# Performance work log

Measured on AMD Instinct MI355X. Metric: run time of the kernel, lower is better.

Reference implementation:

```python
import math
import jax, jax.numpy as jnp
import numpy as np

B, N, L, D, H = 1, 64, 512, 768, 12
DK = D // H


def setup_inputs() -> dict:
    rng = jax.random.key(0)
    ks = jax.random.split(rng, 8)
    s = 0.02  # weight init scale
    return {
        "query": jax.random.normal(ks[0], (B, N, L, D), jnp.float32),
        "key": jax.random.normal(ks[1], (B, N, L, D), jnp.float32),
        "value": jax.random.normal(ks[2], (B, N, L, D), jnp.float32),
        "Wq": jax.random.normal(ks[3], (D, D), jnp.float32) * s,
        "bq": jnp.zeros((D,), jnp.float32),
        "Wk": jax.random.normal(ks[4], (D, D), jnp.float32) * s,
        "bk": jnp.zeros((D,), jnp.float32),
        "Wv": jax.random.normal(ks[5], (D, D), jnp.float32) * s,
        "bv": jnp.zeros((D,), jnp.float32),
        "Wo": jax.random.normal(ks[6], (D, D), jnp.float32) * s,
        "bo": jnp.zeros((D,), jnp.float32),
    }


def reference(query, key, value, Wq, bq, Wk, bk, Wv, bv, Wo, bo):
    b, n, l, d = query.shape
    h, dk = H, DK
    # combined scaling: 1/sqrt(d_k) * 1/sqrt(N)
    scale = 1.0 / (math.sqrt(dk) * math.sqrt(n))
    # nn.Linear: y = x @ W.T + b  (W is [out, in])
    q = (jnp.einsum('bnld,ed->bnle', query, Wq) + bq).reshape(b, n, l, h, dk) * scale
    k = (jnp.einsum('bnld,ed->bnle', key, Wk) + bk).reshape(b, n, l, h, dk)
    v = (jnp.einsum('bnld,ed->bnle', value, Wv) + bv).reshape(b, n, l, h, dk)
    # tied attention: scores summed over the N (sequence-copy) axis BEFORE softmax
    att = jnp.einsum('bnihk,bnjhk->bhij', q, k)  # [B,H,L,L]
    att = jax.nn.softmax(att, axis=-1)  # dropout is identity in eval
    # single attention map broadcast across all N value tensors
    out = jnp.einsum('bhij,bnjhk->bnihk', att, v).reshape(b, n, l, d)
    return jnp.einsum('bnld,ed->bnle', out, Wo) + bo
```

## Files before the change

kernel.cpp:

```cpp
#include <hip/hip_runtime.h>


typedef __bf16 bf16x8 __attribute__((ext_vector_type(8)));
typedef float f32x4 __attribute__((ext_vector_type(4)));

__device__ __forceinline__ unsigned short f2bf(float f) {
  unsigned u = __float_as_uint(f);
  u += 0x7fffu + ((u >> 16) & 1u);
  return (unsigned short)(u >> 16);
}

__device__ __forceinline__ void gll16(const unsigned short* g, unsigned short* l) {
  __builtin_amdgcn_global_load_lds(
      (const __attribute__((address_space(1))) unsigned int*)g,
      (__attribute__((address_space(3))) unsigned int*)l, 16, 0, 0);
}

enum { MODE_QCAT = 0, MODE_VT = 1, MODE_ATT = 2, MODE_OUTWS = 3, MODE_OUT_BIAS = 4 };

constexpr int BM = 128, BN = 128, BK = 32;

template <int MODE, bool SWZ, int KS>
__global__ __launch_bounds__(256, 2) void gemm_bt(
    const void* __restrict__ Av, const void* __restrict__ Bv,
    const float* __restrict__ bias, void* __restrict__ Cv,
    int K, int lda, int ldb, long long a_bs, long long b_bs,
    float alpha, int ntn,
    const float* __restrict__ bias2, float alpha2, long long c_bs) {
  constexpr int LP = 32;

  __shared__ unsigned short As[BM * LP];
  __shared__ unsigned short Bs[BN * LP];

  const int tid = threadIdx.x;
  const int wave = tid >> 6;
  const int lane = tid & 63;
  const int wm = wave >> 1, wn = wave & 1;

  int tm, tn, batch = 0, ks = 0;
  if constexpr (SWZ && MODE == MODE_ATT) {
    const int bid = blockIdx.x;
    const int xcd = bid & 7, j = bid >> 3;
    const int z = (j >> 4) * 8 + xcd;
    const int tile = j & 15;
    tn = tile & 3;
    tm = tile >> 2;
    ks = z % KS;
    batch = z / KS;
  } else if constexpr (SWZ && MODE == MODE_OUTWS) {
    const int bid = blockIdx.x;
    const int xcd = bid & 7, j = bid >> 3;
    const int g = (j >> 6) * 8 + xcd;
    const int idx = j & 63;
    batch = g >> 1;
    tm = idx >> 4;
    tn = (g & 1) * 16 + (idx & 15);
  } else {
    if constexpr (SWZ) {
      const int bid = blockIdx.x;
      const int xcd = bid & 7;
      const int k = bid >> 3;
      tn = k % ntn;
      tm = (k / ntn) * 8 + xcd;
    } else {
      tn = blockIdx.x;
      tm = blockIdx.y;
    }
    batch = blockIdx.z;
    if constexpr (KS > 1) { ks = batch % KS; batch /= KS; }
  }

  const long long m0 = (long long)tm * BM;
  const long long n0 = (long long)tn * BN;

  const unsigned short* Ab = (const unsigned short*)Av + (long long)batch * a_bs + (long long)ks * K;
  const unsigned short* Bb = (const unsigned short*)Bv + (long long)batch * b_bs + (long long)ks * K;

  f32x4 acc[4][4] = {};

  const int l15 = lane & 15;
  const int kq = (lane >> 4) * 8;
  const int r_in = lane >> 2;
  const int c8 = (lane & 3) * 8;

  for (int k0 = 0; k0 < K; k0 += BK) {
#pragma unroll
    for (int t = 0; t < 2; ++t) {
      const int rb = t * 64 + wave * 16;
      gll16((const unsigned short*)Ab + (m0 + rb + r_in) * (long long)lda + k0 + c8,
            &As[rb * LP]);
      gll16((const unsigned short*)Bb + (n0 + rb + r_in) * (long long)ldb + k0 + c8,
            &Bs[rb * LP]);
    }
    __syncthreads();

    bf16x8 af[4], bfr[4];
#pragma unroll
    for (int t = 0; t < 4; ++t)
      af[t] = *(const bf16x8*)&As[(wm * 64 + t * 16 + l15) * LP + kq];
#pragma unroll
    for (int u = 0; u < 4; ++u)
      bfr[u] = *(const bf16x8*)&Bs[(wn * 64 + u * 16 + l15) * LP + kq];
#pragma unroll
    for (int t = 0; t < 4; ++t)
#pragma unroll
      for (int u = 0; u < 4; ++u)
        acc[t][u] = __builtin_amdgcn_mfma_f32_16x16x32_bf16(af[t], bfr[u], acc[t][u], 0, 0, 0);
    __syncthreads();
  }

#pragma unroll
  for (int t = 0; t < 4; ++t) {
#pragma unroll
    for (int u = 0; u < 4; ++u) {
      const long long col = n0 + wn * 64 + u * 16 + l15;
#pragma unroll
      for (int r = 0; r < 4; ++r) {
        const long long row = m0 + wm * 64 + t * 16 + (lane >> 4) * 4 + r;
        float v = acc[t][u][r];
        if constexpr (MODE == MODE_QCAT) {
          const float* bb = batch ? bias2 : bias;
          const float aa = batch ? alpha2 : alpha;
          v = (v + bb[col]) * aa;
          const long long h = col >> 6, kk = col & 63, n = row >> 9, i = row & 511;
          ((unsigned short*)Cv + batch * c_bs)[((h * 512 + i) << 12) + (n << 6) + kk] = f2bf(v);
        } else if constexpr (MODE == MODE_VT) {
          v = v + bias[col];
          const long long h = col >> 6, kk = col & 63, n = row >> 9, j = row & 511;
          ((unsigned short*)Cv)[(((h << 12) + (n << 6) + kk) << 9) + j] = f2bf(v);
        } else if constexpr (MODE == MODE_ATT) {
          float* p = &((float*)Cv)[((long long)batch << 18) + (row << 9) + col];
          if constexpr (KS > 1) atomicAdd(p, v); else *p = v;
        } else if constexpr (MODE == MODE_OUTWS) {
          const long long n = col >> 6, kk = col & 63;
          ((unsigned short*)Cv)[(n * 512 + row) * 768 + (long long)batch * 64 + kk] = f2bf(v);
        } else {
          ((float*)Cv)[row * 768 + col] = v + bias[col];
        }
      }
    }
  }
}

__global__ __launch_bounds__(256) void softmax_rows(const float* __restrict__ att,
                                                    unsigned short* __restrict__ outb) {
  const long long rowbase = (long long)blockIdx.x << 9;
  const int tid = threadIdx.x;
  float a = att[rowbase + tid];
  float b = att[rowbase + tid + 256];

  float m = fmaxf(a, b);
#pragma unroll
  for (int off = 32; off; off >>= 1) m = fmaxf(m, __shfl_down(m, off));
  __shared__ float redm[4];
  if ((tid & 63) == 0) redm[tid >> 6] = m;
  __syncthreads();
  m = fmaxf(fmaxf(redm[0], redm[1]), fmaxf(redm[2], redm[3]));

  const float e0 = __expf(a - m), e1 = __expf(b - m);
  float s = e0 + e1;
#pragma unroll
  for (int off = 32; off; off >>= 1) s += __shfl_down(s, off);
  __shared__ float reds[4];
  if ((tid & 63) == 0) reds[tid >> 6] = s;
  __syncthreads();
  s = reds[0] + reds[1] + reds[2] + reds[3];

  const float inv = 1.0f / s;
  outb[rowbase + tid] = f2bf(e0 * inv);
  outb[rowbase + tid + 256] = f2bf(e1 * inv);
}

__global__ __launch_bounds__(256) void cvt_bf16(const float* __restrict__ in,
                                                unsigned short* __restrict__ out) {
  const long long i = ((long long)blockIdx.x * 256 + threadIdx.x) * 8;
  const float4 a = *(const float4*)(in + i);
  const float4 b = *(const float4*)(in + i + 4);
  uint4 p;
  p.x = (unsigned)f2bf(a.x) | ((unsigned)f2bf(a.y) << 16);
  p.y = (unsigned)f2bf(a.z) | ((unsigned)f2bf(a.w) << 16);
  p.z = (unsigned)f2bf(b.x) | ((unsigned)f2bf(b.y) << 16);
  p.w = (unsigned)f2bf(b.z) | ((unsigned)f2bf(b.w) << 16);
  *(uint4*)(out + i) = p;
}

__global__ __launch_bounds__(256) void cvt_qk(
    const float* __restrict__ s0, const float* __restrict__ s1,
    unsigned short* __restrict__ d0, unsigned short* __restrict__ d1) {
  const float* s = blockIdx.y ? s1 : s0;
  unsigned short* d = blockIdx.y ? d1 : d0;
  const long long i = ((long long)blockIdx.x * 256 + threadIdx.x) * 8;
  const float4 a = *(const float4*)(s + i);
  const float4 b = *(const float4*)(s + i + 4);
  uint4 p;
  p.x = (unsigned)f2bf(a.x) | ((unsigned)f2bf(a.y) << 16);
  p.y = (unsigned)f2bf(a.z) | ((unsigned)f2bf(a.w) << 16);
  p.z = (unsigned)f2bf(b.x) | ((unsigned)f2bf(b.y) << 16);
  p.w = (unsigned)f2bf(b.z) | ((unsigned)f2bf(b.w) << 16);
  *(uint4*)(d + i) = p;
}

__global__ __launch_bounds__(256) void cvt_w4(
    const float* __restrict__ s0, const float* __restrict__ s1,
    const float* __restrict__ s2, const float* __restrict__ s3,
    unsigned short* __restrict__ d0, unsigned short* __restrict__ d1,
    unsigned short* __restrict__ d2, unsigned short* __restrict__ d3) {
  const float* s;
  unsigned short* d;
  switch (blockIdx.y) {
    case 0: s = s0; d = d0; break;
    case 1: s = s1; d = d1; break;
    case 2: s = s2; d = d2; break;
    default: s = s3; d = d3; break;
  }
  const long long i = ((long long)blockIdx.x * 256 + threadIdx.x) * 8;
  const float4 a = *(const float4*)(s + i);
  const float4 b = *(const float4*)(s + i + 4);
  uint4 p;
  p.x = (unsigned)f2bf(a.x) | ((unsigned)f2bf(a.y) << 16);
  p.y = (unsigned)f2bf(a.z) | ((unsigned)f2bf(a.w) << 16);
  p.z = (unsigned)f2bf(b.x) | ((unsigned)f2bf(b.y) << 16);
  p.w = (unsigned)f2bf(b.z) | ((unsigned)f2bf(b.w) << 16);
  *(uint4*)(d + i) = p;
}

extern "C" void kernel_launch(void* const* d_in, const int* in_sizes, int n_in,
                              void* d_out, int out_size, void* d_ws, size_t ws_size,
                              hipStream_t stream) {
  const float* query = (const float*)d_in[0];
  const float* key   = (const float*)d_in[1];
  const float* value = (const float*)d_in[2];
  const float* Wq = (const float*)d_in[3];
  const float* bq = (const float*)d_in[4];
  const float* Wk = (const float*)d_in[5];
  const float* bk = (const float*)d_in[6];
  const float* Wv = (const float*)d_in[7];
  const float* bv = (const float*)d_in[8];
  const float* Wo = (const float*)d_in[9];
  const float* bo = (const float*)d_in[10];
  float* out = (float*)d_out;

  char* ws = (char*)d_ws;
  unsigned short* q_ws  = (unsigned short*)(ws);
  unsigned short* k_ws  = (unsigned short*)(ws + 50331648);
  unsigned short* vt_ws = (unsigned short*)(ws + 100663296);
  float*          att   = (float*)(ws + 150994944);
  unsigned short* wo_b  = (unsigned short*)(ws + 163577856);
  unsigned short* wq_b  = (unsigned short*)(ws + 150994944);
  unsigned short* wk_b  = (unsigned short*)(ws + 150994944 + 1179648);
  unsigned short* wv_b  = (unsigned short*)(ws + 150994944 + 2359296);
  unsigned short* att_b = k_ws;
  unsigned short* out_ws = q_ws;
  unsigned short* xb0 = (unsigned short*)d_out;
  unsigned short* xb1 = (unsigned short*)d_out + 25165824;

  const dim3 blk(256);

  cvt_w4<<<dim3(288, 4), blk, 0, stream>>>(Wo, Wq, Wk, Wv, wo_b, wq_b, wk_b, wv_b);

  cvt_qk<<<dim3(12288, 2), blk, 0, stream>>>(query, key, xb0, xb1);

  gemm_bt<MODE_QCAT, true, 1><<<dim3(1536, 1, 2), blk, 0, stream>>>(
      xb0, wq_b, bq, q_ws, 768, 768, 768, 25165824LL, 589824LL, 0.015625f, 6,
      bk, 1.0f, 25165824LL);

  cvt_bf16<<<12288, blk, 0, stream>>>(value, xb0);
  gemm_bt<MODE_VT, true, 1><<<dim3(1536, 1, 1), blk, 0, stream>>>(
      xb0, wv_b, bv, vt_ws, 768, 768, 768, 0, 0, 1.0f, 6, nullptr, 0.0f, 0);

  hipMemsetAsync(att, 0, 12582912, stream);
  gemm_bt<MODE_ATT, true, 4><<<dim3(768, 1, 1), blk, 0, stream>>>(
      q_ws, k_ws, nullptr, att, 1024, 4096, 4096, 2097152LL, 2097152LL, 1.0f, 0,
      nullptr, 0.0f, 0);

  softmax_rows<<<6144, blk, 0, stream>>>(att, att_b);

  gemm_bt<MODE_OUTWS, true, 1><<<dim3(1536, 1, 1), blk, 0, stream>>>(
      att_b, vt_ws, nullptr, out_ws, 512, 512, 512, 262144LL, 2097152LL, 1.0f, 0,
      nullptr, 0.0f, 0);

  gemm_bt<MODE_OUT_BIAS, true, 1><<<dim3(1536, 1, 1), blk, 0, stream>>>(
      out_ws, wo_b, bo, out, 768, 768, 768, 0, 0, 1.0f, 6, nullptr, 0.0f, 0);
}
```

Before: 668.2 us.

## Double-buffer LDS tiles in GEMM with manual vmcnt waits to overlap loads

Splits the shared-memory tiles into two buffers and software-pipelines the K loop. The next tile is issued with global_load_lds while MFMAs run on the current one, and explicit s_waitcnt vmcnt plus barriers control completion. This hides global load latency that the single-buffer loop exposed before each compute step. It also hoists bias loads out of the epilogue. LDS use doubles, which may cut occupancy at 2 blocks per CU, and the loop assumes K is a multiple of 64.

```diff
diff --git a/kernel.cpp b/kernel.cpp
--- a/kernel.cpp
+++ b/kernel.cpp
@@ -15,6 +15,10 @@
       (const __attribute__((address_space(1))) unsigned int*)g,
       (__attribute__((address_space(3))) unsigned int*)l, 16, 0, 0);
 }
+
+#define VMCNT_4 asm volatile("s_waitcnt vmcnt(4)" ::: "memory")
+#define VMCNT_0 asm volatile("s_waitcnt vmcnt(0)" ::: "memory")
+#define BAR __builtin_amdgcn_s_barrier()
 
 enum { MODE_QCAT = 0, MODE_VT = 1, MODE_ATT = 2, MODE_OUTWS = 3, MODE_OUT_BIAS = 4 };
 
@@ -29,8 +33,10 @@
     const float* __restrict__ bias2, float alpha2, long long c_bs) {
   constexpr int LP = 32;
 
-  __shared__ unsigned short As[BM * LP];
-  __shared__ unsigned short Bs[BN * LP];
+  __shared__ unsigned short As0[BM * LP];
+  __shared__ unsigned short Bs0[BN * LP];
+  __shared__ unsigned short As1[BM * LP];
+  __shared__ unsigned short Bs1[BN * LP];
 
   const int tid = threadIdx.x;
   const int wave = tid >> 6;
@@ -83,30 +89,61 @@
   const int r_in = lane >> 2;
   const int c8 = (lane & 3) * 8;
 
-  for (int k0 = 0; k0 < K; k0 += BK) {
+  auto stage = [&](unsigned short* Asb, unsigned short* Bsb, int k0) {
 #pragma unroll
     for (int t = 0; t < 2; ++t) {
       const int rb = t * 64 + wave * 16;
-      gll16((const unsigned short*)Ab + (m0 + rb + r_in) * (long long)lda + k0 + c8,
-            &As[rb * LP]);
-      gll16((const unsigned short*)Bb + (n0 + rb + r_in) * (long long)ldb + k0 + c8,
-            &Bs[rb * LP]);
+      gll16(Ab + (m0 + rb + r_in) * (long long)lda + k0 + c8, &Asb[rb * LP]);
+      gll16(Bb + (n0 + rb + r_in) * (long long)ldb + k0 + c8, &Bsb[rb * LP]);
     }
-    __syncthreads();
-
+  };
+  auto compute = [&](const unsigned short* Asb, const unsigned short* Bsb) {
     bf16x8 af[4], bfr[4];
 #pragma unroll
     for (int t = 0; t < 4; ++t)
-      af[t] = *(const bf16x8*)&As[(wm * 64 + t * 16 + l15) * LP + kq];
+      af[t] = *(const bf16x8*)&Asb[(wm * 64 + t * 16 + l15) * LP + kq];
 #pragma unroll
     for (int u = 0; u < 4; ++u)
-      bfr[u] = *(const bf16x8*)&Bs[(wn * 64 + u * 16 + l15) * LP + kq];
+      bfr[u] = *(const bf16x8*)&Bsb[(wn * 64 + u * 16 + l15) * LP + kq];
 #pragma unroll
     for (int t = 0; t < 4; ++t)
 #pragma unroll
       for (int u = 0; u < 4; ++u)
         acc[t][u] = __builtin_amdgcn_mfma_f32_16x16x32_bf16(af[t], bfr[u], acc[t][u], 0, 0, 0);
-    __syncthreads();
+  };
+
+  float bpre[4] = {};
+  float aa = alpha;
+  if constexpr (MODE == MODE_QCAT) {
+    const float* bb = batch ? bias2 : bias;
+    aa = batch ? alpha2 : alpha;
+#pragma unroll
+    for (int u = 0; u < 4; ++u) bpre[u] = bb[n0 + wn * 64 + u * 16 + l15];
+  } else if constexpr (MODE == MODE_VT || MODE == MODE_OUT_BIAS) {
+#pragma unroll
+    for (int u = 0; u < 4; ++u) bpre[u] = bias[n0 + wn * 64 + u * 16 + l15];
+  }
+
+  stage(As0, Bs0, 0);
+  VMCNT_0;
+  BAR;
+
+  const int NT = K >> 5;
+  for (int t = 0; t < NT; t += 2) {
+    stage(As1, Bs1, (t + 1) << 5);
+    VMCNT_4;
+    BAR;
+    compute(As0, Bs0);
+    BAR;
+    if (t + 2 < NT) {
+      stage(As0, Bs0, (t + 2) << 5);
+      VMCNT_4;
+    } else {
+      VMCNT_0;
+    }
+    BAR;
+    compute(As1, Bs1);
+    BAR;
   }
 
 #pragma unroll
@@ -119,13 +156,11 @@
         const long long row = m0 + wm * 64 + t * 16 + (lane >> 4) * 4 + r;
         float v = acc[t][u][r];
         if constexpr (MODE == MODE_QCAT) {
-          const float* bb = batch ? bias2 : bias;
-          const float aa = batch ? alpha2 : alpha;
-          v = (v + bb[col]) * aa;
+          v = (v + bpre[u]) * aa;
           const long long h = col >> 6, kk = col & 63, n = row >> 9, i = row & 511;
           ((unsigned short*)Cv + batch * c_bs)[((h * 512 + i) << 12) + (n << 6) + kk] = f2bf(v);
         } else if constexpr (MODE == MODE_VT) {
-          v = v + bias[col];
+          v = v + bpre[u];
           const long long h = col >> 6, kk = col & 63, n = row >> 9, j = row & 511;
           ((unsigned short*)Cv)[(((h << 12) + (n << 6) + kk) << 9) + j] = f2bf(v);
         } else if constexpr (MODE == MODE_ATT) {
@@ -135,7 +170,7 @@
           const long long n = col >> 6, kk = col & 63;
           ((unsigned short*)Cv)[(n * 512 + row) * 768 + (long long)batch * 64 + kk] = f2bf(v);
         } else {
-          ((float*)Cv)[row * 768 + col] = v + bias[col];
+          ((float*)Cv)[row * 768 + col] = v + bpre[u];
         }
       }
     }
```

New measurement: 643.3 us. -3.7%, faster.
